# Performance work log

Hardware: AMD Instinct MI355X
Metric: run time of the kernel (lower is better)

The kernel has to match this reference:

```python
import jax, jax.numpy as jnp
import numpy as np
from jax import lax

SPATIAL = 4
DN = ('NCHW', 'OIHW', 'NCHW')

def setup_inputs() -> dict:
    key = jax.random.key(0)
    ks = jax.random.split(key, 6)
    b, c_in, h, w = 32, 256, 56, 56
    c_out, kk, n_exp, red = 256, 3, 3, 16
    fan = c_in * kk * kk
    return {
        'x': jax.random.normal(ks[0], (b, c_in, h, w), jnp.float32),
        'w_expert': jax.random.normal(ks[1], (n_exp, c_out, c_in, kk, kk), jnp.float32) / np.sqrt(fan),
        'route_conv_w': jax.random.normal(ks[2], (red, c_in), jnp.float32) / np.sqrt(c_in),
        'route_conv_b': jax.random.normal(ks[3], (red,), jnp.float32) * 0.05,
        'fc_w': jax.random.normal(ks[4], (n_exp, red * SPATIAL * SPATIAL), jnp.float32) / np.sqrt(red * SPATIAL * SPATIAL),
        'fc_b': jax.random.normal(ks[5], (n_exp,), jnp.float32) * 0.05,
    }

def _routing(x, route_conv_w, route_conv_b, fc_w, fc_b):
    b, c, h, w = x.shape
    # AdaptiveAvgPool2d(4): h, w divisible by 4 -> exact block mean
    pooled = x.reshape(b, c, SPATIAL, h // SPATIAL, SPATIAL, w // SPATIAL).mean(axis=(3, 5))  # [b,c,4,4]
    r = jnp.einsum('bcij,rc->brij', pooled, route_conv_w) + route_conv_b[None, :, None, None]
    r = jax.nn.relu(r).reshape(b, -1)                         # [b, red*16]
    r = jax.nn.relu(r @ fc_w.T + fc_b)                        # [b, n_exp]
    return jax.nn.sigmoid(r)

def reference(x, w_expert, route_conv_w, route_conv_b, fc_w, fc_b):
    rw = _routing(x, route_conv_w, route_conv_b, fc_w, fc_b)              # [b,k]
    cw = jnp.einsum('bk,koihw->boihw', rw, w_expert)                      # per-sample mixed weights
    def conv1(xi, wi):
        return lax.conv_general_dilated(xi[None], wi, window_strides=(1, 1),
                                        padding=[(1, 1), (1, 1)],
                                        dimension_numbers=DN)[0]
    return jax.vmap(conv1)(x, cw)  # [b, c_out, h, w]
```

## Files before the change

### kernel.cpp

```cpp
#include <hip/hip_runtime.h>
#include <hip/hip_bf16.h>
#include <stdint.h>

#define NB   32
#define CIN  256
#define COUT 256
#define WW   56
#define HW   3136
#define NEXP 3
#define KTOT 2304
#define XP   58
#define XPP  3364
#define NKT  36

typedef __attribute__((ext_vector_type(8))) __bf16 bf16x8;
typedef __attribute__((ext_vector_type(4))) float  f32x4;

#define OFF_RW     0
#define OFF_POOLED 1024
#define OFF_CWT    (1024 + 32*256*16*4)
#define CWT_BYTES  ((size_t)NB*COUT*KTOT*2)
#define OFF_XPAD   (OFF_CWT + CWT_BYTES)

#define PRE_XPAD 6272
#define PRE_POOL 8192
#define PRE_NBLK (PRE_XPAD + PRE_POOL + NB)

__global__ __launch_bounds__(256) void k_pre(const float* __restrict__ x,
                                             float* __restrict__ pooled,
                                             __bf16* __restrict__ xpad) {
    __shared__ __align__(16) char smem[8448];
    int blk = blockIdx.x;
    int t = threadIdx.x;

    if (blk < PRE_XPAD) {
        int pt = blk % 49;
        int r2 = blk / 49;
        int ct = r2 & 3;
        int b  = r2 >> 2;
        __bf16 (*lds)[66] = (__bf16(*)[66])smem;
        int pl = t & 63;
        int cb = t >> 6;
        const float* xb = x + ((size_t)(b * CIN + ct * 64)) * HW + pt * 64;
        #pragma unroll
        for (int ic = 0; ic < 16; ++ic) {
            int cl = ic * 4 + cb;
            lds[cl][pl] = (__bf16)xb[(size_t)cl * HW + pl];
        }
        __syncthreads();
        #pragma unroll
        for (int iw = 0; iw < 2; ++iw) {
            int idx = iw * 256 + t;
            int p_l = idx >> 3, c8 = (idx & 7) * 8;
            int p = pt * 64 + p_l;
            int y = p / WW, xx = p - y * WW;
            union { __bf16 h[8]; uint4 u; } pk;
            #pragma unroll
            for (int j = 0; j < 8; ++j) pk.h[j] = lds[c8 + j][p_l];
            __bf16* dst = xpad + ((size_t)b * XPP + (y + 1) * XP + (xx + 1)) * CIN
                          + ct * 64 + c8;
            *(uint4*)dst = pk.u;
        }
    } else if (blk < PRE_XPAD + PRE_POOL) {
        int j = blk - PRE_XPAD;
        int b = j >> 8, c = j & 255;
        float (*lds)[56] = (float(*)[56])smem;
        const float* xb = x + ((size_t)(b * CIN + c)) * HW;
        if (t < 224) {
            int xc = t % 56, yg = t / 56;
            const float* p = xb + (yg * 14) * WW + xc;
            float s = 0.f;
            #pragma unroll
            for (int r = 0; r < 14; ++r) s += p[r * WW];
            lds[yg][xc] = s;
        }
        __syncthreads();
        if (t < 16) {
            int sy = t >> 2, sx = t & 3;
            float s = 0.f;
            #pragma unroll
            for (int jj = 0; jj < 14; ++jj) s += lds[sy][sx * 14 + jj];
            pooled[(((size_t)b * CIN + c) << 4) + t] = s * (1.f / 196.f);
        }
    } else {
        int b = blk - (PRE_XPAD + PRE_POOL);
        for (int idx = t; idx < 228 * 32; idx += 256) {
            int pos = idx >> 5;
            int co = (idx & 31) * 8;
            int yy, xx;
            if (pos < 58)       { yy = 0;          xx = pos; }
            else if (pos < 116) { yy = 57;         xx = pos - 58; }
            else if (pos < 172) { yy = pos - 115;  xx = 0; }
            else                { yy = pos - 171;  xx = 57; }
            uint4 z = {0u, 0u, 0u, 0u};
            *(uint4*)(xpad + ((size_t)b * XPP + yy * XP + xx) * CIN + co) = z;
        }
    }
}

__global__ __launch_bounds__(256) void k_route(const float* __restrict__ pooled,
                                               const float* __restrict__ rcw,
                                               const float* __restrict__ rcb,
                                               const float* __restrict__ fcw,
                                               const float* __restrict__ fcb,
                                               float* __restrict__ rw) {
    int b = blockIdx.x;
    int t = threadIdx.x;
    int r = t >> 4, ij = t & 15;
    __shared__ float rbuf[256];
    const float* pb = pooled + (size_t)b * CIN * 16;
    float acc = rcb[r];
    for (int c = 0; c < CIN; ++c)
        acc += pb[c * 16 + ij] * rcw[r * CIN + c];
    rbuf[t] = fmaxf(acc, 0.f);
    __syncthreads();
    if (t < NEXP) {
        float a = fcb[t];
        for (int f = 0; f < 256; ++f) a += rbuf[f] * fcw[t * 256 + f];
        a = fmaxf(a, 0.f);
        rw[b * NEXP + t] = 1.f / (1.f + expf(-a));
    }
}

__global__ __launch_bounds__(256) void k_mixw(const float* __restrict__ we,
                                              const float* __restrict__ rw,
                                              __bf16* __restrict__ cwt) {
    int o = blockIdx.x;
    int i = threadIdx.x;
    float wv[3][9];
    #pragma unroll
    for (int e = 0; e < 3; ++e) {
        const float* p = we + (((size_t)e * COUT + o) * CIN + i) * 9;
        #pragma unroll
        for (int k = 0; k < 9; ++k) wv[e][k] = p[k];
    }
    for (int b = 0; b < NB; ++b) {
        float r0 = rw[b * 3 + 0], r1 = rw[b * 3 + 1], r2 = rw[b * 3 + 2];
        __bf16* op = cwt + ((size_t)(b * COUT + o)) * KTOT + i;
        #pragma unroll
        for (int k = 0; k < 9; ++k) {
            float v = r0 * wv[0][k] + r1 * wv[1][k] + r2 * wv[2][k];
            op[k * 256] = (__bf16)v;
        }
    }
}

#define GL16(g, l) __builtin_amdgcn_global_load_lds( \
    (const __attribute__((address_space(1))) uint32_t*)(g), \
    (__attribute__((address_space(3))) uint32_t*)(l), 16, 0, 0)

#define STAGE_A(o, kh, aoffn) do { \
    GL16(gA0 + (aoffn) + (kh)*64, LDS + (o)*32768 + (kh)*16384 + wid*1024); \
    GL16(gA1 + (aoffn) + (kh)*64, LDS + (o)*32768 + (kh)*16384 + 8192 + wid*1024); \
  } while (0)
#define STAGE_B(o, kh, boffn) do { \
    GL16(gB0 + (boffn) + (kh)*64, LDS + 65536 + (o)*32768 + (kh)*16384 + wid*1024); \
    GL16(gB1 + (boffn) + (kh)*64, LDS + 65536 + (o)*32768 + (kh)*16384 + 8192 + wid*1024); \
  } while (0)

#define BARRIER() do { \
    __builtin_amdgcn_sched_barrier(0); \
    __builtin_amdgcn_s_barrier(); \
    __builtin_amdgcn_sched_barrier(0); \
  } while (0)
#define VMCNT(n) do { \
    asm volatile("s_waitcnt vmcnt(" #n ")" ::: "memory"); \
    __builtin_amdgcn_sched_barrier(0); \
  } while (0)

#define LOADA(aCur, kh, q) do { \
    af[0] = *(const bf16x8*)((aCur) + (kh)*16384 + (q)*4096 + 0); \
    af[1] = *(const bf16x8*)((aCur) + (kh)*16384 + (q)*4096 + 1024); \
    af[2] = *(const bf16x8*)((aCur) + (kh)*16384 + (q)*4096 + 2048); \
    af[3] = *(const bf16x8*)((aCur) + (kh)*16384 + (q)*4096 + 3072); \
  } while (0)
#define LOADB(bCur, kh) do { \
    bq[0] = *(const bf16x8*)((bCur) + (kh)*16384 + 0); \
    bq[1] = *(const bf16x8*)((bCur) + (kh)*16384 + 1024); \
    bq[2] = *(const bf16x8*)((bCur) + (kh)*16384 + 2048); \
    bq[3] = *(const bf16x8*)((bCur) + (kh)*16384 + 3072); \
  } while (0)
#define LGKM0() do { \
    asm volatile("s_waitcnt lgkmcnt(0)" ::: "memory"); \
    __builtin_amdgcn_sched_barrier(0); \
  } while (0)
#define MM(qb) do { \
    __builtin_amdgcn_s_setprio(1); \
    _Pragma("unroll") \
    for (int mf = 0; mf < 4; ++mf) \
      _Pragma("unroll") \
      for (int nf = 0; nf < 4; ++nf) \
        acc[(qb) + mf][nf] = __builtin_amdgcn_mfma_f32_16x16x32_bf16( \
            af[mf], bq[nf], acc[(qb) + mf][nf], 0, 0, 0); \
    __builtin_amdgcn_s_setprio(0); \
  } while (0)

__global__ __launch_bounds__(512, 2) void k_conv(const __bf16* __restrict__ cwt,
                                                 const __bf16* __restrict__ xpad,
                                                 float* __restrict__ out) {
    extern __shared__ __align__(16) char LDS[];

    int flat = blockIdx.x;
    int logical = (flat & 7) * 52 + (flat >> 3);
    int b  = logical / 13;
    int nt = logical - b * 13;

    int tid = threadIdx.x;
    int ln  = tid & 63;
    int wid = tid >> 6;
    int wr  = wid >> 2;
    int wc  = wid & 3;
    int fr  = ln & 15;
    int kw  = ln >> 4;
    int xsw = ((fr >> 1) & 3) << 4;

    const char *gA0, *gA1, *gB0, *gB1;
    {
        const char* cwb = (const char*)(cwt + (size_t)b * COUT * KTOT);
        const char* xpb = (const char*)(xpad + (size_t)b * XPP * CIN);
        #pragma unroll
        for (int i = 0; i < 2; ++i) {
            int L = i * 8192 + wid * 1024 + ln * 16;
            int U = L ^ (((L >> 7) & 3) << 4);
            int rowU = U >> 6;
            int kbU  = U & 63;
            const char* ga = cwb + (size_t)rowU * (KTOT * 2) + kbU;
            int p = nt * 256 + rowU; if (p > HW - 1) p = HW - 1;
            int y = p / WW, x = p - y * WW;
            const char* gb = xpb + (size_t)(y * XP + x) * (CIN * 2) + kbU;
            if (i == 0) { gA0 = ga; gB0 = gb; } else { gA1 = ga; gB1 = gb; }
        }
    }

    int aRd = (wr * 128 + fr) * 64 + ((kw * 16) ^ xsw);
    int bRd = (wc * 64 + fr) * 64 + ((kw * 16) ^ xsw);

    f32x4 acc[8][4];
    #pragma unroll
    for (int i = 0; i < 8; ++i)
        #pragma unroll
        for (int j = 0; j < 4; ++j)
            acc[i][j] = (f32x4){0.f, 0.f, 0.f, 0.f};

    bf16x8 af[4], bq[4];

    STAGE_A(0, 0, 0);
    STAGE_B(0, 0, 0);
    STAGE_A(0, 1, 0);
    STAGE_B(0, 1, 0);

    for (int kt = 0; kt < NKT - 1; ++kt) {
        int c = kt & 1, o = c ^ 1;
        int ktn  = kt + 1;
        int aoffn = ktn * 128;
        int ktap = ktn >> 2;
        int kyn  = (ktap * 11) >> 5;
        int kxn  = ktap - kyn * 3;
        int boffn = (kyn * XP + kxn) * 512 + (ktn & 3) * 128;
        const char* aCur = LDS + c * 32768 + aRd;
        const char* bCur = LDS + 65536 + c * 32768 + bRd;

        VMCNT(4);
        BARRIER();
        LOADA(aCur, 0, 0);
        LOADB(bCur, 0);
        STAGE_A(o, 0, aoffn);
        LGKM0();
        MM(0);
        LOADA(aCur, 0, 1);
        STAGE_B(o, 0, boffn);
        LGKM0();
        MM(4);
        VMCNT(4);
        BARRIER();
        LOADA(aCur, 1, 0);
        LOADB(bCur, 1);
        STAGE_A(o, 1, aoffn);
        LGKM0();
        MM(0);
        LOADA(aCur, 1, 1);
        STAGE_B(o, 1, boffn);
        LGKM0();
        MM(4);
    }

    {
        VMCNT(0);
        BARRIER();
        const char* aCur = LDS + 32768 + aRd;
        const char* bCur = LDS + 65536 + 32768 + bRd;
        LOADA(aCur, 0, 0); LOADB(bCur, 0); LGKM0(); MM(0);
        LOADA(aCur, 0, 1);                 LGKM0(); MM(4);
        LOADA(aCur, 1, 0); LOADB(bCur, 1); LGKM0(); MM(0);
        LOADA(aCur, 1, 1);                 LGKM0(); MM(4);
    }

    float* ob = out + ((size_t)(b * COUT + wr * 128)) * HW;
    int colbase = nt * 256 + wc * 64;
    int rb = (ln >> 4) * 4;
    #pragma unroll
    for (int q = 0; q < 2; ++q)
        #pragma unroll
        for (int nf = 0; nf < 4; ++nf) {
            int col = colbase + nf * 16 + fr;
            if (col < HW) {
                #pragma unroll
                for (int mf = 0; mf < 4; ++mf)
                    #pragma unroll
                    for (int r = 0; r < 4; ++r)
                        ob[(size_t)(q * 64 + mf * 16 + rb + r) * HW + col] =
                            acc[q * 4 + mf][nf][r];
            }
        }
}

extern "C" void kernel_launch(void* const* d_in, const int* in_sizes, int n_in,
                              void* d_out, int out_size, void* d_ws, size_t ws_size,
                              hipStream_t stream) {
    (void)in_sizes; (void)n_in; (void)out_size; (void)ws_size;
    const float* x   = (const float*)d_in[0];
    const float* we  = (const float*)d_in[1];
    const float* rcw = (const float*)d_in[2];
    const float* rcb = (const float*)d_in[3];
    const float* fcw = (const float*)d_in[4];
    const float* fcb = (const float*)d_in[5];
    float* out = (float*)d_out;

    char* ws = (char*)d_ws;
    float*  rw     = (float*)(ws + OFF_RW);
    float*  pooled = (float*)(ws + OFF_POOLED);
    __bf16* cwt    = (__bf16*)(ws + OFF_CWT);
    __bf16* xpad   = (__bf16*)(ws + OFF_XPAD);

    (void)hipFuncSetAttribute((const void*)k_conv,
                              hipFuncAttributeMaxDynamicSharedMemorySize, 131072);

    k_pre<<<PRE_NBLK, 256, 0, stream>>>(x, pooled, xpad);
    k_route<<<NB, 256, 0, stream>>>(pooled, rcw, rcb, fcw, fcb, rw);
    k_mixw<<<COUT, 256, 0, stream>>>(we, rw, cwt);
    k_conv<<<416, 512, 131072, stream>>>(cwt, xpad, out);
}
```

Before: 196.8 us.

## Fuse pooling into transpose pass and restructure conv inner loop LDS loads

Avoids a second full read of x by accumulating the adaptive-average-pool sums during the bf16 transpose/pad pass. Partial sums go into shared-memory atomics and then into global atomics, which needs a memset of pooled beforehand; the 1/196 scale moves into the routing kernel. The conv main loop is also reorganised: each half-step issues both global stages first, then loads all A and B fragments into separate registers and runs 32 MFMAs back to back. This uses more VGPRs, and the atomics make the pooling sum order nondeterministic.

```diff
diff --git a/kernel.cpp b/kernel.cpp
--- a/kernel.cpp
+++ b/kernel.cpp
@@ -21,15 +21,16 @@
 #define OFF_CWT    (1024 + 32*256*16*4)
 #define CWT_BYTES  ((size_t)NB*COUT*KTOT*2)
 #define OFF_XPAD   (OFF_CWT + CWT_BYTES)
+#define POOLED_BYTES (32*256*16*4)
 
 #define PRE_XPAD 6272
-#define PRE_POOL 8192
-#define PRE_NBLK (PRE_XPAD + PRE_POOL + NB)
+#define PRE_NBLK (PRE_XPAD + NB)
 
 __global__ __launch_bounds__(256) void k_pre(const float* __restrict__ x,
                                              float* __restrict__ pooled,
                                              __bf16* __restrict__ xpad) {
-    __shared__ __align__(16) char smem[8448];
+    __shared__ __align__(16) __bf16 lds[64][66];
+    __shared__ float pbuf[64][16];
     int blk = blockIdx.x;
     int t = threadIdx.x;
 
@@ -38,52 +39,43 @@
         int r2 = blk / 49;
         int ct = r2 & 3;
         int b  = r2 >> 2;
-        __bf16 (*lds)[66] = (__bf16(*)[66])smem;
         int pl = t & 63;
         int cb = t >> 6;
+        for (int i = t; i < 1024; i += 256) ((float*)pbuf)[i] = 0.f;
+        __syncthreads();
+        int p  = pt * 64 + pl;
+        int y  = p / WW, xx = p - y * WW;
+        int cell = (y / 14) * 4 + (xx / 14);
         const float* xb = x + ((size_t)(b * CIN + ct * 64)) * HW + pt * 64;
         #pragma unroll
         for (int ic = 0; ic < 16; ++ic) {
             int cl = ic * 4 + cb;
-            lds[cl][pl] = (__bf16)xb[(size_t)cl * HW + pl];
+            float v = xb[(size_t)cl * HW + pl];
+            lds[cl][pl] = (__bf16)v;
+            atomicAdd(&pbuf[cl][cell], v);
         }
         __syncthreads();
         #pragma unroll
         for (int iw = 0; iw < 2; ++iw) {
             int idx = iw * 256 + t;
             int p_l = idx >> 3, c8 = (idx & 7) * 8;
-            int p = pt * 64 + p_l;
-            int y = p / WW, xx = p - y * WW;
+            int pp = pt * 64 + p_l;
+            int yy = pp / WW, xq = pp - yy * WW;
             union { __bf16 h[8]; uint4 u; } pk;
             #pragma unroll
             for (int j = 0; j < 8; ++j) pk.h[j] = lds[c8 + j][p_l];
-            __bf16* dst = xpad + ((size_t)b * XPP + (y + 1) * XP + (xx + 1)) * CIN
+            __bf16* dst = xpad + ((size_t)b * XPP + (yy + 1) * XP + (xq + 1)) * CIN
                           + ct * 64 + c8;
             *(uint4*)dst = pk.u;
         }
-    } else if (blk < PRE_XPAD + PRE_POOL) {
-        int j = blk - PRE_XPAD;
-        int b = j >> 8, c = j & 255;
-        float (*lds)[56] = (float(*)[56])smem;
-        const float* xb = x + ((size_t)(b * CIN + c)) * HW;
-        if (t < 224) {
-            int xc = t % 56, yg = t / 56;
-            const float* p = xb + (yg * 14) * WW + xc;
-            float s = 0.f;
-            #pragma unroll
-            for (int r = 0; r < 14; ++r) s += p[r * WW];
-            lds[yg][xc] = s;
-        }
-        __syncthreads();
-        if (t < 16) {
-            int sy = t >> 2, sx = t & 3;
-            float s = 0.f;
-            #pragma unroll
-            for (int jj = 0; jj < 14; ++jj) s += lds[sy][sx * 14 + jj];
-            pooled[(((size_t)b * CIN + c) << 4) + t] = s * (1.f / 196.f);
+        for (int i = t; i < 1024; i += 256) {
+            float v = ((float*)pbuf)[i];
+            if (v != 0.f)
+                atomicAdd(&pooled[(((size_t)b * CIN + ct * 64 + (i >> 4)) << 4)
+                                  + (i & 15)], v);
         }
     } else {
-        int b = blk - (PRE_XPAD + PRE_POOL);
+        int b = blk - PRE_XPAD;
         for (int idx = t; idx < 228 * 32; idx += 256) {
             int pos = idx >> 5;
             int co = (idx & 31) * 8;
@@ -109,9 +101,10 @@
     int r = t >> 4, ij = t & 15;
     __shared__ float rbuf[256];
     const float* pb = pooled + (size_t)b * CIN * 16;
-    float acc = rcb[r];
+    float acc = 0.f;
     for (int c = 0; c < CIN; ++c)
         acc += pb[c * 16 + ij] * rcw[r * CIN + c];
+    acc = acc * (1.f / 196.f) + rcb[r];
     rbuf[t] = fmaxf(acc, 0.f);
     __syncthreads();
     if (t < NEXP) {
@@ -167,31 +160,40 @@
     asm volatile("s_waitcnt vmcnt(" #n ")" ::: "memory"); \
     __builtin_amdgcn_sched_barrier(0); \
   } while (0)
-
-#define LOADA(aCur, kh, q) do { \
-    af[0] = *(const bf16x8*)((aCur) + (kh)*16384 + (q)*4096 + 0); \
-    af[1] = *(const bf16x8*)((aCur) + (kh)*16384 + (q)*4096 + 1024); \
-    af[2] = *(const bf16x8*)((aCur) + (kh)*16384 + (q)*4096 + 2048); \
-    af[3] = *(const bf16x8*)((aCur) + (kh)*16384 + (q)*4096 + 3072); \
-  } while (0)
-#define LOADB(bCur, kh) do { \
-    bq[0] = *(const bf16x8*)((bCur) + (kh)*16384 + 0); \
-    bq[1] = *(const bf16x8*)((bCur) + (kh)*16384 + 1024); \
-    bq[2] = *(const bf16x8*)((bCur) + (kh)*16384 + 2048); \
-    bq[3] = *(const bf16x8*)((bCur) + (kh)*16384 + 3072); \
-  } while (0)
 #define LGKM0() do { \
     asm volatile("s_waitcnt lgkmcnt(0)" ::: "memory"); \
     __builtin_amdgcn_sched_barrier(0); \
   } while (0)
-#define MM(qb) do { \
-    __builtin_amdgcn_s_setprio(1); \
+
+#define LOADF(F, base, kh, q) do { \
+    F[0] = *(const bf16x8*)((base) + (kh)*16384 + (q)*4096 + 0); \
+    F[1] = *(const bf16x8*)((base) + (kh)*16384 + (q)*4096 + 1024); \
+    F[2] = *(const bf16x8*)((base) + (kh)*16384 + (q)*4096 + 2048); \
+    F[3] = *(const bf16x8*)((base) + (kh)*16384 + (q)*4096 + 3072); \
+  } while (0)
+#define MM(qb, F) do { \
     _Pragma("unroll") \
     for (int mf = 0; mf < 4; ++mf) \
       _Pragma("unroll") \
       for (int nf = 0; nf < 4; ++nf) \
         acc[(qb) + mf][nf] = __builtin_amdgcn_mfma_f32_16x16x32_bf16( \
-            af[mf], bq[nf], acc[(qb) + mf][nf], 0, 0, 0); \
+            F[mf], bq[nf], acc[(qb) + mf][nf], 0, 0, 0); \
+  } while (0)
+
+#define HALF(c, o, kh, aoffn, boffn) do { \
+    VMCNT(4); \
+    BARRIER(); \
+    STAGE_A(o, kh, aoffn); \
+    STAGE_B(o, kh, boffn); \
+    { const char* aCur = LDS + (c) * 32768 + aRd; \
+      const char* bCur = LDS + 65536 + (c) * 32768 + bRd; \
+      LOADF(af, aCur, kh, 0); \
+      LOADF(bq, bCur, kh, 0); \
+      LOADF(ag, aCur, kh, 1); } \
+    LGKM0(); \
+    __builtin_amdgcn_s_setprio(1); \
+    MM(0, af); \
+    MM(4, ag); \
     __builtin_amdgcn_s_setprio(0); \
   } while (0)
 
@@ -242,7 +244,7 @@
         for (int j = 0; j < 4; ++j)
             acc[i][j] = (f32x4){0.f, 0.f, 0.f, 0.f};
 
-    bf16x8 af[4], bq[4];
+    bf16x8 af[4], ag[4], bq[4];
 
     STAGE_A(0, 0, 0);
     STAGE_B(0, 0, 0);
@@ -257,31 +259,9 @@
         int kyn  = (ktap * 11) >> 5;
         int kxn  = ktap - kyn * 3;
         int boffn = (kyn * XP + kxn) * 512 + (ktn & 3) * 128;
-        const char* aCur = LDS + c * 32768 + aRd;
-        const char* bCur = LDS + 65536 + c * 32768 + bRd;
-
-        VMCNT(4);
-        BARRIER();
-        LOADA(aCur, 0, 0);
-        LOADB(bCur, 0);
-        STAGE_A(o, 0, aoffn);
-        LGKM0();
-        MM(0);
-        LOADA(aCur, 0, 1);
-        STAGE_B(o, 0, boffn);
-        LGKM0();
-        MM(4);
-        VMCNT(4);
-        BARRIER();
-        LOADA(aCur, 1, 0);
-        LOADB(bCur, 1);
-        STAGE_A(o, 1, aoffn);
-        LGKM0();
-        MM(0);
-        LOADA(aCur, 1, 1);
-        STAGE_B(o, 1, boffn);
-        LGKM0();
-        MM(4);
+
+        HALF(c, o, 0, aoffn, boffn);
+        HALF(c, o, 1, aoffn, boffn);
     }
 
     {
@@ -289,10 +269,14 @@
         BARRIER();
         const char* aCur = LDS + 32768 + aRd;
         const char* bCur = LDS + 65536 + 32768 + bRd;
-        LOADA(aCur, 0, 0); LOADB(bCur, 0); LGKM0(); MM(0);
-        LOADA(aCur, 0, 1);                 LGKM0(); MM(4);
-        LOADA(aCur, 1, 0); LOADB(bCur, 1); LGKM0(); MM(0);
-        LOADA(aCur, 1, 1);                 LGKM0(); MM(4);
+        LOADF(af, aCur, 0, 0); LOADF(bq, bCur, 0, 0); LOADF(ag, aCur, 0, 1);
+        LGKM0();
+        __builtin_amdgcn_s_setprio(1); MM(0, af); MM(4, ag);
+        __builtin_amdgcn_s_setprio(0);
+        LOADF(af, aCur, 1, 0); LOADF(bq, bCur, 1, 0); LOADF(ag, aCur, 1, 1);
+        LGKM0();
+        __builtin_amdgcn_s_setprio(1); MM(0, af); MM(4, ag);
+        __builtin_amdgcn_s_setprio(0);
     }
 
     float* ob = out + ((size_t)(b * COUT + wr * 128)) * HW;
@@ -335,6 +319,7 @@
     (void)hipFuncSetAttribute((const void*)k_conv,
                               hipFuncAttributeMaxDynamicSharedMemorySize, 131072);
 
+    (void)hipMemsetAsync(pooled, 0, POOLED_BYTES, stream);
     k_pre<<<PRE_NBLK, 256, 0, stream>>>(x, pooled, xpad);
     k_route<<<NB, 256, 0, stream>>>(pooled, rcw, rcb, fcw, fcb, rw);
     k_mixw<<<COUT, 256, 0, stream>>>(we, rw, cwt);
```

New measurement: 335.1 us. 70.3% more time.
